# Kernel optimization log

Measured on AMD Instinct MI355X. Metric: run time of the kernel, lower is better.

The kernel has to match this reference:

```python
import jax, jax.numpy as jnp
import numpy as np

ALPHA, BETA, GAMMA = 0.5, 0.003, 0.001
NUM_CLASSES = 1000
NUM_FEATURES = 1000
BATCH = 16384


def setup_inputs() -> dict:
    key = jax.random.key(0)
    k1, k2, k3 = jax.random.split(key, 3)
    x = jax.random.normal(k1, (BATCH, NUM_FEATURES), dtype=jnp.float32)
    y = jax.random.randint(k2, (BATCH,), 0, NUM_CLASSES)
    centers = jax.random.normal(k3, (NUM_CLASSES, NUM_FEATURES), dtype=jnp.float32)
    return {"x": x, "y": y, "centers": centers}


def reference(x, y, centers):
    B = x.shape[0]
    C = NUM_CLASSES
    # cross entropy (x used as logits, as in nn.CrossEntropyLoss)
    logp = jax.nn.log_softmax(x, axis=-1)
    ce = -jnp.mean(jnp.take_along_axis(logp, y[:, None], axis=1))
    # center loss on PRE-update centers
    c_y = centers[y]                       # [B, F]
    delta = x - c_y
    center_loss = jnp.mean(jnp.sum(delta * delta, axis=1))
    # functional form of the in-place per-class center update:
    # centers[i] += alpha * mean(delta[y == i])
    counts = jax.ops.segment_sum(jnp.ones((B,), x.dtype), y, num_segments=C)  # [C]
    sum_delta = jax.ops.segment_sum(delta, y, num_segments=C)                 # [C, F]
    mean_delta = jnp.where(counts[:, None] > 0,
                           sum_delta / jnp.maximum(counts, 1)[:, None],
                           jnp.zeros_like(sum_delta))
    new_centers = centers + ALPHA * mean_delta
    # inter loss: sum_{i<j} ||c_i - c_j||^2 = C*sum_i||c_i||^2 - ||sum_i c_i||^2
    sq = jnp.sum(new_centers * new_centers, axis=1)   # [C]
    s = jnp.sum(new_centers, axis=0)                  # [F]
    num_pairs = C * (C - 1) / 2
    inter_loss = (C * jnp.sum(sq) - jnp.sum(s * s)) / num_pairs
    # intra loss on POST-update centers: mean over class, averaged over classes
    d2 = jnp.sum((x - new_centers[y]) ** 2, axis=1)   # [B]
    per_class_sum = jax.ops.segment_sum(d2, y, num_segments=C)
    per_class_mean = jnp.where(counts > 0, per_class_sum / jnp.maximum(counts, 1),
                               jnp.zeros_like(per_class_sum))
    intra_loss = jnp.sum(per_class_mean) / C
    return ce + BETA * center_loss + GAMMA * inter_loss + GAMMA * intra_loss
```

## Files before the change

### kernel.cpp

```cpp
#include <hip/hip_runtime.h>
#include <math.h>

#define NF 1000
#define NC 1000
#define NB 16384
#define NV 250
#define ALPHA_C 0.5f
#define BETA_C 0.003f
#define GAMMA_C 0.001f
#define MAXL 512

__device__ __forceinline__ float wave_sum(float v) {
#pragma unroll
    for (int off = 32; off > 0; off >>= 1) v += __shfl_xor(v, off, 64);
    return v;
}
__device__ __forceinline__ float wave_max(float v) {
#pragma unroll
    for (int off = 32; off > 0; off >>= 1) v = fmaxf(v, __shfl_xor(v, off, 64));
    return v;
}

__global__ __launch_bounds__(256) void row_pass(
    const float* __restrict__ x, const int* __restrict__ y,
    const float* __restrict__ centers,
    float* __restrict__ ce, float* __restrict__ d2) {
    const int wid = threadIdx.x >> 6, lane = threadIdx.x & 63;
    const int b = blockIdx.x * 4 + wid;
    const int cls = y[b];
    const float4* xrow = (const float4*)(x + (size_t)b * NF);
    const float4* crow = (const float4*)(centers + (size_t)cls * NF);

    float4 xv[4], cv[4];
#pragma unroll
    for (int i = 0; i < 4; i++) {
        int idx = lane + i * 64;
        if (idx < NV) {
            xv[i] = xrow[idx];
            cv[i] = crow[idx];
        } else {
            xv[i] = make_float4(-INFINITY, -INFINITY, -INFINITY, -INFINITY);
            cv[i] = make_float4(0.f, 0.f, 0.f, 0.f);
        }
    }
    const float xy = x[(size_t)b * NF + cls];

    float lmax = -INFINITY;
#pragma unroll
    for (int i = 0; i < 4; i++)
        lmax = fmaxf(fmaxf(fmaxf(lmax, xv[i].x), fmaxf(xv[i].y, xv[i].z)), xv[i].w);
    const float rmax = wave_max(lmax);

    float lsum = 0.f, ld2 = 0.f;
#pragma unroll
    for (int i = 0; i < 4; i++) {
        int idx = lane + i * 64;
        lsum += expf(xv[i].x - rmax) + expf(xv[i].y - rmax) +
                expf(xv[i].z - rmax) + expf(xv[i].w - rmax);
        if (idx < NV) {
            float dx = xv[i].x - cv[i].x, dy = xv[i].y - cv[i].y;
            float dz = xv[i].z - cv[i].z, dw = xv[i].w - cv[i].w;
            ld2 += dx * dx + dy * dy + dz * dz + dw * dw;
        }
    }
    const float sumexp = wave_sum(lsum);
    const float rd2 = wave_sum(ld2);
    if (lane == 0) {
        ce[b] = -(xy - rmax - logf(sumexp));
        d2[b] = rd2;
    }
}

__global__ __launch_bounds__(256) void class_pass(
    const float* __restrict__ x, const int* __restrict__ y,
    const float* __restrict__ centers,
    const float* __restrict__ ce, const float* __restrict__ d2,
    float* __restrict__ new_centers, float4* __restrict__ partials) {
    __shared__ float sb[16];
    __shared__ int list[MAXL];
    __shared__ int lcount;
    const int c = blockIdx.x, t = threadIdx.x;
    if (t == 0) lcount = 0;
    __syncthreads();

    const int4* y4 = (const int4*)y;
    for (int i = t; i < NB / 4; i += 256) {
        int4 v = y4[i];
        int b = 4 * i;
        if (v.x == c) { int p = atomicAdd(&lcount, 1); list[p & (MAXL - 1)] = b; }
        if (v.y == c) { int p = atomicAdd(&lcount, 1); list[p & (MAXL - 1)] = b + 1; }
        if (v.z == c) { int p = atomicAdd(&lcount, 1); list[p & (MAXL - 1)] = b + 2; }
        if (v.w == c) { int p = atomicAdd(&lcount, 1); list[p & (MAXL - 1)] = b + 3; }
    }
    __syncthreads();
    const int n = lcount;

    float lce = 0.f, ld2 = 0.f;
    for (int j = t; j < n; j += 256) {
        int b = list[j];
        lce += ce[b];
        ld2 += d2[b];
    }

    float4 a0 = make_float4(0, 0, 0, 0), a1 = make_float4(0, 0, 0, 0);
    float4 a2 = make_float4(0, 0, 0, 0), a3 = make_float4(0, 0, 0, 0);
    if (t < NV) {
        int i = 0;
        for (; i + 3 < n; i += 4) {
            const float4 v0 = ((const float4*)(x + (size_t)list[i + 0] * NF))[t];
            const float4 v1 = ((const float4*)(x + (size_t)list[i + 1] * NF))[t];
            const float4 v2 = ((const float4*)(x + (size_t)list[i + 2] * NF))[t];
            const float4 v3 = ((const float4*)(x + (size_t)list[i + 3] * NF))[t];
            a0.x += v0.x; a0.y += v0.y; a0.z += v0.z; a0.w += v0.w;
            a1.x += v1.x; a1.y += v1.y; a1.z += v1.z; a1.w += v1.w;
            a2.x += v2.x; a2.y += v2.y; a2.z += v2.z; a2.w += v2.w;
            a3.x += v3.x; a3.y += v3.y; a3.z += v3.z; a3.w += v3.w;
        }
        for (; i < n; i++) {
            const float4 v0 = ((const float4*)(x + (size_t)list[i] * NF))[t];
            a0.x += v0.x; a0.y += v0.y; a0.z += v0.z; a0.w += v0.w;
        }
    }
    a0.x += a1.x + a2.x + a3.x; a0.y += a1.y + a2.y + a3.y;
    a0.z += a1.z + a2.z + a3.z; a0.w += a1.w + a2.w + a3.w;

    const float inv = (n > 0) ? 1.f / (float)n : 0.f;
    float lsq = 0.f, lmd2 = 0.f;
    if (t < NV) {
        float4 cv = ((const float4*)(centers + (size_t)c * NF))[t];
        float4 md, nc;
        md.x = (n > 0) ? (a0.x * inv - cv.x) : 0.f;
        md.y = (n > 0) ? (a0.y * inv - cv.y) : 0.f;
        md.z = (n > 0) ? (a0.z * inv - cv.z) : 0.f;
        md.w = (n > 0) ? (a0.w * inv - cv.w) : 0.f;
        nc.x = cv.x + ALPHA_C * md.x; nc.y = cv.y + ALPHA_C * md.y;
        nc.z = cv.z + ALPHA_C * md.z; nc.w = cv.w + ALPHA_C * md.w;
        ((float4*)(new_centers + (size_t)c * NF))[t] = nc;
        lsq = nc.x * nc.x + nc.y * nc.y + nc.z * nc.z + nc.w * nc.w;
        lmd2 = md.x * md.x + md.y * md.y + md.z * md.z + md.w * md.w;
    }

    float w0 = wave_sum(lsq), w1 = wave_sum(lmd2), w2 = wave_sum(lce), w3 = wave_sum(ld2);
    const int wid = t >> 6, lane = t & 63;
    if (lane == 0) { sb[wid] = w0; sb[4 + wid] = w1; sb[8 + wid] = w2; sb[12 + wid] = w3; }
    __syncthreads();
    if (t == 0) {
        float sq  = sb[0] + sb[1] + sb[2] + sb[3];
        float md2 = sb[4] + sb[5] + sb[6] + sb[7];
        float ces = sb[8] + sb[9] + sb[10] + sb[11];
        float s2  = sb[12] + sb[13] + sb[14] + sb[15];
        float intra = (n > 0) ? (s2 * inv - ALPHA_C * (2.f - ALPHA_C) * md2) : 0.f;
        partials[c] = make_float4(ces, s2, sq, intra);
    }
}

__global__ __launch_bounds__(256) void col_partial(
    const float* __restrict__ new_centers, float* __restrict__ s_part) {
    const int f = blockIdx.x * 256 + threadIdx.x;
    if (f >= NF) return;
    float acc = 0.f;
    for (int c = blockIdx.y; c < NC; c += gridDim.y)
        acc += new_centers[(size_t)c * NF + f];
    s_part[blockIdx.y * NF + f] = acc;
}

__global__ __launch_bounds__(1024) void finalize(
    const float* __restrict__ s_part, const float4* __restrict__ partials,
    float* __restrict__ out) {
    __shared__ float sb[80];
    const int t = threadIdx.x;
    float ssq = 0.f, ces = 0.f, s2 = 0.f, sq = 0.f, intra = 0.f;
    if (t < NC) {
        float s = 0.f;
#pragma unroll
        for (int k = 0; k < 16; k++) s += s_part[k * NF + t];
        ssq = s * s;
        float4 p = partials[t];
        ces = p.x; s2 = p.y; sq = p.z; intra = p.w;
    }
    float w0 = wave_sum(ssq), w1 = wave_sum(ces), w2 = wave_sum(s2);
    float w3 = wave_sum(sq), w4 = wave_sum(intra);
    const int wid = t >> 6, lane = t & 63;
    if (lane == 0) {
        sb[wid] = w0; sb[16 + wid] = w1; sb[32 + wid] = w2;
        sb[48 + wid] = w3; sb[64 + wid] = w4;
    }
    __syncthreads();
    if (t == 0) {
        float Sssq = 0.f, Sces = 0.f, Ss2 = 0.f, Ssq = 0.f, Sintra = 0.f;
        for (int k = 0; k < 16; k++) {
            Sssq += sb[k]; Sces += sb[16 + k]; Ss2 += sb[32 + k];
            Ssq += sb[48 + k]; Sintra += sb[64 + k];
        }
        float cem = Sces / (float)NB;
        float cl = Ss2 / (float)NB;
        float num_pairs = (float)NC * (float)(NC - 1) * 0.5f;
        float inter = ((float)NC * Ssq - Sssq) / num_pairs;
        float intra_l = Sintra / (float)NC;
        out[0] = cem + BETA_C * cl + GAMMA_C * inter + GAMMA_C * intra_l;
    }
}

extern "C" void kernel_launch(void* const* d_in, const int* in_sizes, int n_in,
                              void* d_out, int out_size, void* d_ws, size_t ws_size,
                              hipStream_t stream) {
    const float* x = (const float*)d_in[0];
    const int* y = (const int*)d_in[1];
    const float* centers = (const float*)d_in[2];
    float* out = (float*)d_out;

    char* ws = (char*)d_ws;
    float* ce          = (float*)(ws);
    float* d2          = (float*)(ws + 65536);
    float* s_part      = (float*)(ws + 131072);
    float4* partials   = (float4*)(ws + 195072);
    float* new_centers = (float*)(ws + 211072);

    row_pass<<<NB / 4, 256, 0, stream>>>(x, y, centers, ce, d2);
    class_pass<<<NC, 256, 0, stream>>>(x, y, centers, ce, d2,
                                       new_centers, partials);
    dim3 cgrid(4, 16);
    col_partial<<<cgrid, 256, 0, stream>>>(new_centers, s_part);
    finalize<<<1, 1024, 0, stream>>>(s_part, partials, out);
}
```

Before: 138.2 us.

## Fuse row-wise softmax/distance pass into per-class gather kernel

Removes the separate per-row kernel and computes log-softmax cross entropy and squared distance to the class center inside the per-class block while its rows are gathered. This avoids reading x twice from memory and drops the intermediate ce/d2 buffers. In exchange each class block processes its rows two at a time with block-wide reductions and several barriers per pair, which serialises work inside a grid of only 1000 blocks.

```diff
diff --git a/kernel.cpp b/kernel.cpp
--- a/kernel.cpp
+++ b/kernel.cpp
@@ -21,65 +21,16 @@
     return v;
 }
 
-__global__ __launch_bounds__(256) void row_pass(
+__global__ __launch_bounds__(256) void class_fused(
     const float* __restrict__ x, const int* __restrict__ y,
     const float* __restrict__ centers,
-    float* __restrict__ ce, float* __restrict__ d2) {
-    const int wid = threadIdx.x >> 6, lane = threadIdx.x & 63;
-    const int b = blockIdx.x * 4 + wid;
-    const int cls = y[b];
-    const float4* xrow = (const float4*)(x + (size_t)b * NF);
-    const float4* crow = (const float4*)(centers + (size_t)cls * NF);
-
-    float4 xv[4], cv[4];
-#pragma unroll
-    for (int i = 0; i < 4; i++) {
-        int idx = lane + i * 64;
-        if (idx < NV) {
-            xv[i] = xrow[idx];
-            cv[i] = crow[idx];
-        } else {
-            xv[i] = make_float4(-INFINITY, -INFINITY, -INFINITY, -INFINITY);
-            cv[i] = make_float4(0.f, 0.f, 0.f, 0.f);
-        }
-    }
-    const float xy = x[(size_t)b * NF + cls];
-
-    float lmax = -INFINITY;
-#pragma unroll
-    for (int i = 0; i < 4; i++)
-        lmax = fmaxf(fmaxf(fmaxf(lmax, xv[i].x), fmaxf(xv[i].y, xv[i].z)), xv[i].w);
-    const float rmax = wave_max(lmax);
-
-    float lsum = 0.f, ld2 = 0.f;
-#pragma unroll
-    for (int i = 0; i < 4; i++) {
-        int idx = lane + i * 64;
-        lsum += expf(xv[i].x - rmax) + expf(xv[i].y - rmax) +
-                expf(xv[i].z - rmax) + expf(xv[i].w - rmax);
-        if (idx < NV) {
-            float dx = xv[i].x - cv[i].x, dy = xv[i].y - cv[i].y;
-            float dz = xv[i].z - cv[i].z, dw = xv[i].w - cv[i].w;
-            ld2 += dx * dx + dy * dy + dz * dz + dw * dw;
-        }
-    }
-    const float sumexp = wave_sum(lsum);
-    const float rd2 = wave_sum(ld2);
-    if (lane == 0) {
-        ce[b] = -(xy - rmax - logf(sumexp));
-        d2[b] = rd2;
-    }
-}
-
-__global__ __launch_bounds__(256) void class_pass(
-    const float* __restrict__ x, const int* __restrict__ y,
-    const float* __restrict__ centers,
-    const float* __restrict__ ce, const float* __restrict__ d2,
     float* __restrict__ new_centers, float4* __restrict__ partials) {
-    __shared__ float sb[16];
     __shared__ int list[MAXL];
     __shared__ int lcount;
+    __shared__ float sb[24];
+    __shared__ float sxy[2];
     const int c = blockIdx.x, t = threadIdx.x;
+    const int wid = t >> 6, lane = t & 63;
     if (t == 0) lcount = 0;
     __syncthreads();
 
@@ -95,62 +46,98 @@
     __syncthreads();
     const int n = lcount;
 
-    float lce = 0.f, ld2 = 0.f;
-    for (int j = t; j < n; j += 256) {
-        int b = list[j];
-        lce += ce[b];
-        ld2 += d2[b];
-    }
-
-    float4 a0 = make_float4(0, 0, 0, 0), a1 = make_float4(0, 0, 0, 0);
-    float4 a2 = make_float4(0, 0, 0, 0), a3 = make_float4(0, 0, 0, 0);
-    if (t < NV) {
-        int i = 0;
-        for (; i + 3 < n; i += 4) {
-            const float4 v0 = ((const float4*)(x + (size_t)list[i + 0] * NF))[t];
-            const float4 v1 = ((const float4*)(x + (size_t)list[i + 1] * NF))[t];
-            const float4 v2 = ((const float4*)(x + (size_t)list[i + 2] * NF))[t];
-            const float4 v3 = ((const float4*)(x + (size_t)list[i + 3] * NF))[t];
-            a0.x += v0.x; a0.y += v0.y; a0.z += v0.z; a0.w += v0.w;
-            a1.x += v1.x; a1.y += v1.y; a1.z += v1.z; a1.w += v1.w;
-            a2.x += v2.x; a2.y += v2.y; a2.z += v2.z; a2.w += v2.w;
-            a3.x += v3.x; a3.y += v3.y; a3.z += v3.z; a3.w += v3.w;
-        }
-        for (; i < n; i++) {
-            const float4 v0 = ((const float4*)(x + (size_t)list[i] * NF))[t];
-            a0.x += v0.x; a0.y += v0.y; a0.z += v0.z; a0.w += v0.w;
-        }
-    }
-    a0.x += a1.x + a2.x + a3.x; a0.y += a1.y + a2.y + a3.y;
-    a0.z += a1.z + a2.z + a3.z; a0.w += a1.w + a2.w + a3.w;
+    float4 cv = make_float4(0.f, 0.f, 0.f, 0.f);
+    if (t < NV) cv = ((const float4*)(centers + (size_t)c * NF))[t];
+    const int xt = c >> 2, xc = c & 3;
+
+    float4 acc = make_float4(0.f, 0.f, 0.f, 0.f);
+    float ce_acc = 0.f, s2_acc = 0.f;
+
+    for (int i = 0; i < n; i += 2) {
+        const bool two = (i + 1 < n);
+        const int b0 = list[i];
+        const int b1 = two ? list[i + 1] : 0;
+        float4 v0, v1;
+        float m0 = -INFINITY, m1 = -INFINITY;
+        if (t < NV) {
+            v0 = ((const float4*)(x + (size_t)b0 * NF))[t];
+            m0 = fmaxf(fmaxf(v0.x, v0.y), fmaxf(v0.z, v0.w));
+            if (two) {
+                v1 = ((const float4*)(x + (size_t)b1 * NF))[t];
+                m1 = fmaxf(fmaxf(v1.x, v1.y), fmaxf(v1.z, v1.w));
+            }
+        }
+        m0 = wave_max(m0);
+        m1 = wave_max(m1);
+        __syncthreads();
+        if (lane == 0) { sb[wid] = m0; sb[4 + wid] = m1; }
+        if (t == xt) {
+            sxy[0] = (xc == 0) ? v0.x : (xc == 1) ? v0.y : (xc == 2) ? v0.z : v0.w;
+            if (two) sxy[1] = (xc == 0) ? v1.x : (xc == 1) ? v1.y : (xc == 2) ? v1.z : v1.w;
+        }
+        __syncthreads();
+        const float rmax0 = fmaxf(fmaxf(sb[0], sb[1]), fmaxf(sb[2], sb[3]));
+        const float rmax1 = fmaxf(fmaxf(sb[4], sb[5]), fmaxf(sb[6], sb[7]));
+
+        float e0 = 0.f, e1 = 0.f, d0 = 0.f, d1 = 0.f;
+        if (t < NV) {
+            e0 = expf(v0.x - rmax0) + expf(v0.y - rmax0) +
+                 expf(v0.z - rmax0) + expf(v0.w - rmax0);
+            float dx = v0.x - cv.x, dy = v0.y - cv.y;
+            float dz = v0.z - cv.z, dw = v0.w - cv.w;
+            d0 = dx * dx + dy * dy + dz * dz + dw * dw;
+            acc.x += v0.x; acc.y += v0.y; acc.z += v0.z; acc.w += v0.w;
+            if (two) {
+                e1 = expf(v1.x - rmax1) + expf(v1.y - rmax1) +
+                     expf(v1.z - rmax1) + expf(v1.w - rmax1);
+                float ex = v1.x - cv.x, ey = v1.y - cv.y;
+                float ez = v1.z - cv.z, ew = v1.w - cv.w;
+                d1 = ex * ex + ey * ey + ez * ez + ew * ew;
+                acc.x += v1.x; acc.y += v1.y; acc.z += v1.z; acc.w += v1.w;
+            }
+        }
+        e0 = wave_sum(e0); e1 = wave_sum(e1);
+        d0 = wave_sum(d0); d1 = wave_sum(d1);
+        if (lane == 0) { sb[8 + wid] = e0; sb[12 + wid] = e1;
+                         sb[16 + wid] = d0; sb[20 + wid] = d1; }
+        __syncthreads();
+        if (t == 0) {
+            float se0 = sb[8] + sb[9] + sb[10] + sb[11];
+            float sd0 = sb[16] + sb[17] + sb[18] + sb[19];
+            ce_acc += -(sxy[0] - rmax0 - logf(se0));
+            s2_acc += sd0;
+            if (two) {
+                float se1 = sb[12] + sb[13] + sb[14] + sb[15];
+                float sd1 = sb[20] + sb[21] + sb[22] + sb[23];
+                ce_acc += -(sxy[1] - rmax1 - logf(se1));
+                s2_acc += sd1;
+            }
+        }
+    }
 
     const float inv = (n > 0) ? 1.f / (float)n : 0.f;
     float lsq = 0.f, lmd2 = 0.f;
     if (t < NV) {
-        float4 cv = ((const float4*)(centers + (size_t)c * NF))[t];
         float4 md, nc;
-        md.x = (n > 0) ? (a0.x * inv - cv.x) : 0.f;
-        md.y = (n > 0) ? (a0.y * inv - cv.y) : 0.f;
-        md.z = (n > 0) ? (a0.z * inv - cv.z) : 0.f;
-        md.w = (n > 0) ? (a0.w * inv - cv.w) : 0.f;
+        md.x = (n > 0) ? (acc.x * inv - cv.x) : 0.f;
+        md.y = (n > 0) ? (acc.y * inv - cv.y) : 0.f;
+        md.z = (n > 0) ? (acc.z * inv - cv.z) : 0.f;
+        md.w = (n > 0) ? (acc.w * inv - cv.w) : 0.f;
         nc.x = cv.x + ALPHA_C * md.x; nc.y = cv.y + ALPHA_C * md.y;
         nc.z = cv.z + ALPHA_C * md.z; nc.w = cv.w + ALPHA_C * md.w;
         ((float4*)(new_centers + (size_t)c * NF))[t] = nc;
         lsq = nc.x * nc.x + nc.y * nc.y + nc.z * nc.z + nc.w * nc.w;
         lmd2 = md.x * md.x + md.y * md.y + md.z * md.z + md.w * md.w;
     }
-
-    float w0 = wave_sum(lsq), w1 = wave_sum(lmd2), w2 = wave_sum(lce), w3 = wave_sum(ld2);
-    const int wid = t >> 6, lane = t & 63;
-    if (lane == 0) { sb[wid] = w0; sb[4 + wid] = w1; sb[8 + wid] = w2; sb[12 + wid] = w3; }
+    float w0 = wave_sum(lsq), w1 = wave_sum(lmd2);
+    __syncthreads();
+    if (lane == 0) { sb[wid] = w0; sb[4 + wid] = w1; }
     __syncthreads();
     if (t == 0) {
-        float sq  = sb[0] + sb[1] + sb[2] + sb[3];
+        float sq = sb[0] + sb[1] + sb[2] + sb[3];
         float md2 = sb[4] + sb[5] + sb[6] + sb[7];
-        float ces = sb[8] + sb[9] + sb[10] + sb[11];
-        float s2  = sb[12] + sb[13] + sb[14] + sb[15];
-        float intra = (n > 0) ? (s2 * inv - ALPHA_C * (2.f - ALPHA_C) * md2) : 0.f;
-        partials[c] = make_float4(ces, s2, sq, intra);
+        float intra = (n > 0) ? (s2_acc * inv - ALPHA_C * (2.f - ALPHA_C) * md2) : 0.f;
+        partials[c] = make_float4(ce_acc, s2_acc, sq, intra);
     }
 }
 
@@ -210,15 +197,11 @@
     float* out = (float*)d_out;
 
     char* ws = (char*)d_ws;
-    float* ce          = (float*)(ws);
-    float* d2          = (float*)(ws + 65536);
-    float* s_part      = (float*)(ws + 131072);
-    float4* partials   = (float4*)(ws + 195072);
-    float* new_centers = (float*)(ws + 211072);
-
-    row_pass<<<NB / 4, 256, 0, stream>>>(x, y, centers, ce, d2);
-    class_pass<<<NC, 256, 0, stream>>>(x, y, centers, ce, d2,
-                                       new_centers, partials);
+    float* s_part      = (float*)(ws);
+    float4* partials   = (float4*)(ws + 64000);
+    float* new_centers = (float*)(ws + 80000);
+
+    class_fused<<<NC, 256, 0, stream>>>(x, y, centers, new_centers, partials);
     dim3 cgrid(4, 16);
     col_partial<<<cgrid, 256, 0, stream>>>(new_centers, s_part);
     finalize<<<1, 1024, 0, stream>>>(s_part, partials, out);
```

Measured after the change: 140.8 us. Within noise of the previous version (+1.9%).
